# Kernel tuning notes

Measured on AMD Instinct MI355X. Metric: run time of the kernel, lower is better.

## Reference

```python
import jax, jax.numpy as jnp
import numpy as np

B, N, DIM = 4, 4096, 512
HEADS, DH = 8, 64          # dim_head = dim // 8
M = 256                    # num_landmarks = dim // 2
ITERS = 6                  # pinv iterations
K = 33                     # residual depthwise conv kernel
INNER = HEADS * DH


def setup_inputs() -> dict:
    key = jax.random.key(0)
    ks = jax.random.split(key, 7)
    return {
        "x": jax.random.normal(ks[0], (B, N, DIM), jnp.float32),
        "norm_w": 1.0 + 0.02 * jax.random.normal(ks[1], (DIM,), jnp.float32),
        "norm_b": 0.02 * jax.random.normal(ks[2], (DIM,), jnp.float32),
        "w_qkv": jax.random.normal(ks[3], (DIM, 3 * INNER), jnp.float32) / np.sqrt(DIM),
        "w_out": jax.random.normal(ks[4], (INNER, DIM), jnp.float32) / np.sqrt(INNER),
        "b_out": 0.02 * jax.random.normal(ks[5], (DIM,), jnp.float32),
        "res_w": jax.random.normal(ks[6], (HEADS, 1, K, 1), jnp.float32) / np.sqrt(K),
    }


def _moore_penrose_pinv(x, iters):
    # iterative Newton-Schulz pseudoinverse, as in lucidrains nystrom-attention
    abs_x = jnp.abs(x)
    col = abs_x.sum(-1)
    row = abs_x.sum(-2)
    z = jnp.swapaxes(x, -1, -2) / (jnp.max(col) * jnp.max(row))
    I = jnp.eye(x.shape[-1], dtype=x.dtype)
    for _ in range(iters):
        xz = x @ z
        z = 0.25 * z @ (13.0 * I - xz @ (15.0 * I - xz @ (7.0 * I - xz)))
    return z


def reference(x, norm_w, norm_b, w_qkv, w_out, b_out, res_w):
    # LayerNorm (eps=1e-5, torch default)
    mu = x.mean(-1, keepdims=True)
    var = ((x - mu) ** 2).mean(-1, keepdims=True)
    xn = (x - mu) / jnp.sqrt(var + 1e-5) * norm_w + norm_b

    qkv = xn @ w_qkv                               # [B,N,3*INNER]
    q, k, v = jnp.split(qkv, 3, axis=-1)
    to_heads = lambda t: t.reshape(B, N, HEADS, DH).transpose(0, 2, 1, 3)  # [B,H,N,D]
    q, k, v = to_heads(q), to_heads(k), to_heads(v)
    q = q * (DH ** -0.5)

    # landmarks: mean over consecutive blocks of l = N // M tokens
    l = N // M
    q_l = q.reshape(B, HEADS, M, l, DH).mean(3)    # [B,H,M,D]
    k_l = k.reshape(B, HEADS, M, l, DH).mean(3)

    sim1 = jnp.einsum('bhid,bhjd->bhij', q, k_l)   # [B,H,N,M]
    sim2 = jnp.einsum('bhid,bhjd->bhij', q_l, k_l) # [B,H,M,M]
    sim3 = jnp.einsum('bhid,bhjd->bhij', q_l, k)   # [B,H,M,N]
    a1 = jax.nn.softmax(sim1, -1)
    a2 = jax.nn.softmax(sim2, -1)
    a3 = jax.nn.softmax(sim3, -1)

    a2_inv = _moore_penrose_pinv(a2, ITERS)
    out = (a1 @ a2_inv) @ (a3 @ v)                 # [B,H,N,D]

    # residual depthwise conv over sequence dim (Conv2d(h,h,(33,1),groups=h))
    out = out + jax.lax.conv_general_dilated(
        v, res_w, (1, 1), ((K // 2, K // 2), (0, 0)),
        feature_group_count=HEADS,
        dimension_numbers=('NCHW', 'OIHW', 'NCHW'))

    out = out.transpose(0, 2, 1, 3).reshape(B, N, INNER)
    out = out @ w_out + b_out                      # to_out (dropout inactive at eval)
    return x + out                                 # TransLayer residual
```

## Files before the change

kernel.cpp:

```cpp
#include <hip/hip_runtime.h>
#include <math.h>

typedef unsigned short u16;
typedef short s16x8 __attribute__((ext_vector_type(8)));
typedef float f32x4 __attribute__((ext_vector_type(4)));

#define MFMA16(a, b, c) __builtin_amdgcn_mfma_f32_16x16x32_bf16((a), (b), (c), 0, 0, 0)

__device__ __forceinline__ u16 f2b(float f) {
  unsigned u = __float_as_uint(f);
  unsigned r = (u + 0x7fff + ((u >> 16) & 1)) >> 16;
  return (u16)r;
}
__device__ __forceinline__ float b2f(u16 h) { return __uint_as_float(((unsigned)h) << 16); }

__global__ __launch_bounds__(256) void ln_kernel(const float* __restrict__ x, const float* __restrict__ w,
                          const float* __restrict__ b, u16* __restrict__ xn) {
  int row = blockIdx.x;
  const float* xr = x + (size_t)row * 512;
  int t = threadIdx.x;
  float v0 = xr[t], v1 = xr[t + 256];
  float s = v0 + v1, ss = v0*v0 + v1*v1;
  for (int o = 32; o > 0; o >>= 1) { s += __shfl_down(s, o); ss += __shfl_down(ss, o); }
  __shared__ float ls[4], lss[4];
  int wid = t >> 6, lane = t & 63;
  if (lane == 0) { ls[wid] = s; lss[wid] = ss; }
  __syncthreads();
  float tot  = ls[0]+ls[1]+ls[2]+ls[3];
  float tot2 = lss[0]+lss[1]+lss[2]+lss[3];
  float mean = tot * (1.f/512);
  float var  = tot2 * (1.f/512) - mean*mean;
  float inv = rsqrtf(var + 1e-5f);
  u16* xo = xn + (size_t)row * 512;
  xo[t]     = f2b((v0-mean)*inv*w[t]     + b[t]);
  xo[t+256] = f2b((v1-mean)*inv*w[t+256] + b[t+256]);
}

__global__ __launch_bounds__(256) void wcast_T(const float* __restrict__ W, u16* __restrict__ WT, int R, int C) {
  int idx = blockIdx.x*256 + threadIdx.x;
  if (idx >= R*C) return;
  int r = idx / C, c = idx - r*C;
  WT[(size_t)c*R + r] = f2b(W[idx]);
}

__global__ __launch_bounds__(256) void vtrans(const u16* __restrict__ v, u16* __restrict__ vT) {
  __shared__ u16 tile[64][72];
  int bh = blockIdx.y, n0 = blockIdx.x * 64;
  int t = threadIdx.x;
  const u16* vb = v + ((size_t)bh*4096 + n0)*64;
  #pragma unroll
  for (int p = 0; p < 2; p++) {
    int c = t + p*256;
    int r = c >> 3, col = (c & 7)*8;
    *(uint4*)&tile[r][col] = *(const uint4*)&vb[(size_t)r*64 + col];
  }
  __syncthreads();
  #pragma unroll
  for (int p = 0; p < 2; p++) {
    int c = t + p*256;
    int d = c >> 3, ncol = (c & 7)*8;
    u16 tmp[8];
    #pragma unroll
    for (int j = 0; j < 8; j++) tmp[j] = tile[ncol + j][d];
    *(uint4*)&vT[((size_t)bh*64 + d)*4096 + n0 + ncol] = *(uint4*)tmp;
  }
}

__device__ __forceinline__ void gemm128_pf(const u16* __restrict__ A, const u16* __restrict__ BT,
    int K, int ldA, int ldBT, int row0, int col0, u16* As, u16* Bs, f32x4 acc[4][4]) {
  int t = threadIdx.x, lane = t & 63, wid = t >> 6;
  int wr = (wid >> 1) * 64, wc = (wid & 1) * 64;
  int lr = lane & 15, lg = lane >> 4;
  int sr = t >> 2, sc = (t & 3) * 8;
  const u16* Ar0 = A  + (size_t)(row0 + sr)*ldA + sc;
  const u16* Ar1 = A  + (size_t)(row0 + sr + 64)*ldA + sc;
  const u16* Br0 = BT + (size_t)(col0 + sr)*ldBT + sc;
  const u16* Br1 = BT + (size_t)(col0 + sr + 64)*ldBT + sc;
  uint4 pa0 = *(const uint4*)Ar0, pa1 = *(const uint4*)Ar1;
  uint4 pb0 = *(const uint4*)Br0, pb1 = *(const uint4*)Br1;
  for (int k0 = 0; k0 < K; k0 += 32) {
    __syncthreads();
    *(uint4*)&As[sr*40 + sc]        = pa0;
    *(uint4*)&As[(sr + 64)*40 + sc] = pa1;
    *(uint4*)&Bs[sr*40 + sc]        = pb0;
    *(uint4*)&Bs[(sr + 64)*40 + sc] = pb1;
    __syncthreads();
    if (k0 + 32 < K) {
      pa0 = *(const uint4*)(Ar0 + k0 + 32);
      pa1 = *(const uint4*)(Ar1 + k0 + 32);
      pb0 = *(const uint4*)(Br0 + k0 + 32);
      pb1 = *(const uint4*)(Br1 + k0 + 32);
    }
    s16x8 af[4], bf[4];
    #pragma unroll
    for (int f = 0; f < 4; f++) {
      af[f] = *(s16x8*)&As[(wr + f*16 + lr)*40 + lg*8];
      bf[f] = *(s16x8*)&Bs[(wc + f*16 + lr)*40 + lg*8];
    }
    #pragma unroll
    for (int i = 0; i < 4; i++)
      #pragma unroll
      for (int j = 0; j < 4; j++)
        acc[i][j] = MFMA16(af[i], bf[j], acc[i][j]);
  }
}

__device__ __forceinline__ void gemm64_pf(const u16* __restrict__ Ab, const u16* __restrict__ Bb,
    int row0, int col0, u16* As, u16* Bs, f32x4 acc[2][2]) {
  int t = threadIdx.x, lane = t & 63, wid = t >> 6;
  int wr = (wid >> 1)*32, wc = (wid & 1)*32;
  int lr = lane & 15, lg = lane >> 4;
  int sr = t >> 3, sc = (t & 7)*8;
  const u16* Ar0 = Ab + (size_t)(row0 + sr)*256 + sc;
  const u16* Ar1 = Ab + (size_t)(row0 + 32 + sr)*256 + sc;
  const u16* Br0 = Bb + (size_t)(col0 + sr)*256 + sc;
  const u16* Br1 = Bb + (size_t)(col0 + 32 + sr)*256 + sc;
  uint4 pa0 = *(const uint4*)Ar0, pa1 = *(const uint4*)Ar1;
  uint4 pb0 = *(const uint4*)Br0, pb1 = *(const uint4*)Br1;
  for (int k0 = 0; k0 < 256; k0 += 64) {
    __syncthreads();
    *(uint4*)&As[sr*72 + sc]        = pa0;
    *(uint4*)&As[(sr + 32)*72 + sc] = pa1;
    *(uint4*)&Bs[sr*72 + sc]        = pb0;
    *(uint4*)&Bs[(sr + 32)*72 + sc] = pb1;
    __syncthreads();
    if (k0 + 64 < 256) {
      pa0 = *(const uint4*)(Ar0 + k0 + 64);
      pa1 = *(const uint4*)(Ar1 + k0 + 64);
      pb0 = *(const uint4*)(Br0 + k0 + 64);
      pb1 = *(const uint4*)(Br1 + k0 + 64);
    }
    #pragma unroll
    for (int kk = 0; kk < 2; kk++) {
      s16x8 af[2], bf[2];
      #pragma unroll
      for (int f = 0; f < 2; f++) {
        af[f] = *(s16x8*)&As[(wr + f*16 + lr)*72 + kk*32 + lg*8];
        bf[f] = *(s16x8*)&Bs[(wc + f*16 + lr)*72 + kk*32 + lg*8];
      }
      #pragma unroll
      for (int i = 0; i < 2; i++)
        #pragma unroll
        for (int j = 0; j < 2; j++)
          acc[i][j] = MFMA16(af[i], bf[j], acc[i][j]);
    }
  }
}

__global__ __launch_bounds__(256, 4) void qkv_mfma(const u16* __restrict__ xn, const u16* __restrict__ wT,
    u16* __restrict__ q, u16* __restrict__ k, u16* __restrict__ v) {
  __shared__ u16 As[128*40], Bs[128*40];
  f32x4 acc[4][4];
  #pragma unroll
  for (int i = 0; i < 4; i++)
    #pragma unroll
    for (int j = 0; j < 4; j++) acc[i][j] = (f32x4)0.f;
  int bI = blockIdx.x;
  int job = (bI & 7)*192 + (bI >> 3);
  int row0 = (job / 12) * 128, col0 = (job % 12) * 128;
  gemm128_pf(xn, wT, 512, 512, 512, row0, col0, As, Bs, acc);
  int t = threadIdx.x, lane = t & 63, wid = t >> 6, lr = lane & 15, lg = lane >> 4;
  int wr = (wid >> 1)*64, wc = (wid & 1)*64;
  #pragma unroll
  for (int i = 0; i < 4; i++)
    #pragma unroll
    for (int j = 0; j < 4; j++)
      #pragma unroll
      for (int r = 0; r < 4; r++) {
        int row = row0 + wr + i*16 + lg*4 + r;
        int col = col0 + wc + j*16 + lr;
        float val = acc[i][j][r];
        int part = col >> 9, rem = col & 511, h = rem >> 6, d = rem & 63;
        int b = row >> 12, n = row & 4095;
        size_t bh = (size_t)(b*8 + h);
        size_t dst = (bh*4096 + n)*64 + d;
        if (part == 0)      q[dst] = f2b(val * 0.125f);
        else if (part == 1) k[dst] = f2b(val);
        else                v[dst] = f2b(val);
      }
}

__global__ __launch_bounds__(256, 4) void out_mfma(const u16* __restrict__ outh, const u16* __restrict__ wT,
    const float* __restrict__ bo, const float* __restrict__ x, float* __restrict__ out) {
  __shared__ u16 As[128*40], Bs[128*40];
  f32x4 acc[4][4];
  #pragma unroll
  for (int i = 0; i < 4; i++)
    #pragma unroll
    for (int j = 0; j < 4; j++) acc[i][j] = (f32x4)0.f;
  int bI = blockIdx.x;
  int job = (bI & 7)*64 + (bI >> 3);
  int row0 = (job / 4) * 128, col0 = (job % 4) * 128;
  gemm128_pf(outh, wT, 512, 512, 512, row0, col0, As, Bs, acc);
  int t = threadIdx.x, lane = t & 63, wid = t >> 6, lr = lane & 15, lg = lane >> 4;
  int wr = (wid >> 1)*64, wc = (wid & 1)*64;
  #pragma unroll
  for (int i = 0; i < 4; i++)
    #pragma unroll
    for (int j = 0; j < 4; j++)
      #pragma unroll
      for (int r = 0; r < 4; r++) {
        int row = row0 + wr + i*16 + lg*4 + r;
        int col = col0 + wc + j*16 + lr;
        size_t idx = (size_t)row*512 + col;
        out[idx] = x[idx] + acc[i][j][r] + bo[col];
      }
}

__global__ __launch_bounds__(256) void pinv_s1(const u16* __restrict__ a2h, const u16* __restrict__ zcT,
    u16* __restrict__ xz, u16* __restrict__ xzT, u16* __restrict__ e1T) {
  __shared__ u16 As[64*72], Bs[64*72];
  size_t bb = (size_t)blockIdx.z << 16;
  f32x4 acc[2][2];
  #pragma unroll
  for (int i = 0; i < 2; i++) { acc[i][0] = (f32x4)0.f; acc[i][1] = (f32x4)0.f; }
  int row0 = blockIdx.y*64, col0 = blockIdx.x*64;
  gemm64_pf(a2h + bb, zcT + bb, row0, col0, As, Bs, acc);
  int t = threadIdx.x, lane = t & 63, wid = t >> 6, lr = lane & 15, lg = lane >> 4;
  int wr = (wid >> 1)*32, wc = (wid & 1)*32;
  #pragma unroll
  for (int i = 0; i < 2; i++)
    #pragma unroll
    for (int j = 0; j < 2; j++)
      #pragma unroll
      for (int r = 0; r < 4; r++) {
        int row = row0 + wr + i*16 + lg*4 + r;
        int col = col0 + wc + j*16 + lr;
        float c = acc[i][j][r];
        xz [bb + (size_t)row*256 + col] = f2b(c);
        xzT[bb + (size_t)col*256 + row] = f2b(c);
        e1T[bb + (size_t)col*256 + row] = f2b((row == col ? 7.f : 0.f) - c);
      }
}

__global__ __launch_bounds__(256) void pinv_s2(const u16* __restrict__ xz, const u16* __restrict__ e1T,
    const u16* __restrict__ zc, const u16* __restrict__ xzT,
    u16* __restrict__ e2T, u16* __restrict__ W) {
  __shared__ u16 As[64*72], Bs[64*72];
  int bz = blockIdx.z;
  bool isQ = bz < 32;
  size_t bb = (size_t)(isQ ? bz : bz - 32) << 16;
  const u16* Aptr = (isQ ? xz : zc) + bb;
  const u16* Bptr = (isQ ? e1T : xzT) + bb;
  f32x4 acc[2][2];
  #pragma unroll
  for (int i = 0; i < 2; i++) { acc[i][0] = (f32x4)0.f; acc[i][1] = (f32x4)0.f; }
  int row0 = blockIdx.y*64, col0 = blockIdx.x*64;
  gemm64_pf(Aptr, Bptr, row0, col0, As, Bs, acc);
  int t = threadIdx.x, lane = t & 63, wid = t >> 6, lr = lane & 15, lg = lane >> 4;
  int wr = (wid >> 1)*32, wc = (wid & 1)*32;
  #pragma unroll
  for (int i = 0; i < 2; i++)
    #pragma unroll
    for (int j = 0; j < 2; j++)
      #pragma unroll
      for (int r = 0; r < 4; r++) {
        int row = row0 + wr + i*16 + lg*4 + r;
        int col = col0 + wc + j*16 + lr;
        float c = acc[i][j][r];
        if (isQ) e2T[bb + (size_t)col*256 + row] = f2b((row == col ? 15.f : 0.f) - c);
        else     W  [bb + (size_t)row*256 + col] = f2b(c);
      }
}

__global__ __launch_bounds__(256) void pinv_s3(const u16* __restrict__ W, const u16* __restrict__ e2T,
    const u16* __restrict__ zc, u16* __restrict__ zn, u16* __restrict__ znT) {
  __shared__ u16 As[64*72], Bs[64*72];
  size_t bb = (size_t)blockIdx.z << 16;
  f32x4 acc[2][2];
  #pragma unroll
  for (int i = 0; i < 2; i++) { acc[i][0] = (f32x4)0.f; acc[i][1] = (f32x4)0.f; }
  int row0 = blockIdx.y*64, col0 = blockIdx.x*64;
  gemm64_pf(W + bb, e2T + bb, row0, col0, As, Bs, acc);
  int t = threadIdx.x, lane = t & 63, wid = t >> 6, lr = lane & 15, lg = lane >> 4;
  int wr = (wid >> 1)*32, wc = (wid & 1)*32;
  #pragma unroll
  for (int i = 0; i < 2; i++)
    #pragma unroll
    for (int j = 0; j < 2; j++)
      #pragma unroll
      for (int r = 0; r < 4; r++) {
        int row = row0 + wr + i*16 + lg*4 + r;
        int col = col0 + wc + j*16 + lr;
        size_t idx = bb + (size_t)row*256 + col;
        float val = 3.25f*b2f(zc[idx]) - 0.25f*acc[i][j][r];
        zn [idx] = f2b(val);
        znT[bb + (size_t)col*256 + row] = f2b(val);
      }
}

__global__ __launch_bounds__(256) void bmm64(const u16* __restrict__ A, const u16* __restrict__ BT,
    u16* __restrict__ CT, int M, int N, int K) {
  __shared__ u16 As[64*40], Bs[64*40];
  int batch = blockIdx.z;
  const u16* Ab = A  + (size_t)batch*M*K;
  const u16* Bb = BT + (size_t)batch*N*K;
  int row0 = blockIdx.y*64, col0 = blockIdx.x*64;
  int t = threadIdx.x, lane = t & 63, wid = t >> 6, lr = lane & 15, lg = lane >> 4;
  int wr = (wid >> 1)*32, wc = (wid & 1)*32;
  int sr = t >> 2, sc = (t & 3)*8;
  const u16* Arow = Ab + (size_t)(row0 + sr)*K + sc;
  const u16* Brow = Bb + (size_t)(col0 + sr)*K + sc;
  uint4 pa = *(const uint4*)Arow;
  uint4 pb = *(const uint4*)Brow;
  f32x4 acc[2][2];
  #pragma unroll
  for (int i = 0; i < 2; i++)
    #pragma unroll
    for (int j = 0; j < 2; j++) acc[i][j] = (f32x4)0.f;
  for (int k0 = 0; k0 < K; k0 += 32) {
    __syncthreads();
    *(uint4*)&As[sr*40 + sc] = pa;
    *(uint4*)&Bs[sr*40 + sc] = pb;
    __syncthreads();
    if (k0 + 32 < K) {
      pa = *(const uint4*)(Arow + k0 + 32);
      pb = *(const uint4*)(Brow + k0 + 32);
    }
    s16x8 af[2], bf[2];
    #pragma unroll
    for (int f = 0; f < 2; f++) {
      af[f] = *(s16x8*)&As[(wr + f*16 + lr)*40 + lg*8];
      bf[f] = *(s16x8*)&Bs[(wc + f*16 + lr)*40 + lg*8];
    }
    #pragma unroll
    for (int i = 0; i < 2; i++)
      #pragma unroll
      for (int j = 0; j < 2; j++)
        acc[i][j] = MFMA16(af[i], bf[j], acc[i][j]);
  }
  size_t cb = (size_t)batch*M*N;
  #pragma unroll
  for (int i = 0; i < 2; i++)
    #pragma unroll
    for (int j = 0; j < 2; j++)
      #pragma unroll
      for (int r = 0; r < 4; r++) {
        int row = row0 + wr + i*16 + lg*4 + r;
        int col = col0 + wc + j*16 + lr;
        CT[cb + (size_t)col*M + row] = f2b(acc[i][j][r]);
      }
}

__global__ void landmark_kernel(const u16* __restrict__ q, const u16* __restrict__ k,
                                u16* __restrict__ ql, u16* __restrict__ kl) {
  int idx = blockIdx.x;
  int d = threadIdx.x;
  size_t base = ((size_t)idx * 16) * 64 + d;
  float sq = 0.f, sk = 0.f;
  #pragma unroll
  for (int j = 0; j < 16; j++) { sq += b2f(q[base + (size_t)j*64]); sk += b2f(k[base + (size_t)j*64]); }
  ql[(size_t)idx*64 + d] = f2b(sq * (1.f/16.f));
  kl[(size_t)idx*64 + d] = f2b(sk * (1.f/16.f));
}

__global__ __launch_bounds__(256, 4) void sim2_mfma(const u16* __restrict__ ql, const u16* __restrict__ kl,
    float* __restrict__ a2, u16* __restrict__ a2h, float* __restrict__ pcs) {
  __shared__ u16 Qs[64*72];
  __shared__ u16 Ks2[256*72];
  __shared__ float wcol[4*256];
  int rq = blockIdx.x, bh = blockIdx.y;
  int t = threadIdx.x, lane = t & 63, wid = t >> 6, lr = lane & 15, lg = lane >> 4;
  #pragma unroll
  for (int p = 0; p < 2; p++) {
    int c = t + p*256;
    int r = c >> 3, col = (c & 7)*8;
    *(uint4*)&Qs[r*72 + col] = *(const uint4*)&ql[((size_t)bh*256 + rq*64 + r)*64 + col];
  }
  #pragma unroll
  for (int p = 0; p < 8; p++) {
    int c = t + p*256;
    int r = c >> 3, col = (c & 7)*8;
    *(uint4*)&Ks2[r*72 + col] = *(const uint4*)&kl[((size_t)bh*256 + r)*64 + col];
  }
  __syncthreads();
  float colp[16];
  #pragma unroll
  for (int cf = 0; cf < 16; cf++) colp[cf] = 0.f;
  int rbase = wid*16;
  s16x8 a0 = *(s16x8*)&Qs[(rbase + lr)*72 + lg*8];
  s16x8 a1 = *(s16x8*)&Qs[(rbase + lr)*72 + 32 + lg*8];
  f32x4 sf[16];
  #pragma unroll
  for (int cf = 0; cf < 16; cf++) {
    s16x8 b0 = *(s16x8*)&Ks2[(cf*16 + lr)*72 + lg*8];
    s16x8 b1 = *(s16x8*)&Ks2[(cf*16 + lr)*72 + 32 + lg*8];
    sf[cf] = MFMA16(a1, b1, MFMA16(a0, b0, (f32x4)0.f));
  }
  #pragma unroll
  for (int r = 0; r < 4; r++) {
    float mx = -3e38f;
    #pragma unroll
    for (int cf = 0; cf < 16; cf++) mx = fmaxf(mx, sf[cf][r]);
    #pragma unroll
    for (int o = 1; o < 16; o <<= 1) mx = fmaxf(mx, __shfl_xor(mx, o));
    float sum = 0.f;
    #pragma unroll
    for (int cf = 0; cf < 16; cf++) { sf[cf][r] = __expf(sf[cf][r] - mx); sum += sf[cf][r]; }
    #pragma unroll
    for (int o = 1; o < 16; o <<= 1) sum += __shfl_xor(sum, o);
    float inv = 1.f / sum;
    int row = rq*64 + rbase + lg*4 + r;
    size_t base = (size_t)bh*65536 + (size_t)row*256;
    #pragma unroll
    for (int cf = 0; cf < 16; cf++) {
      float pp = sf[cf][r] * inv;
      a2[base + cf*16 + lr] = pp;
      a2h[base + cf*16 + lr] = f2b(pp);
      colp[cf] += pp;
    }
  }
  #pragma unroll
  for (int cf = 0; cf < 16; cf++) {
    colp[cf] += __shfl_xor(colp[cf], 16);
    colp[cf] += __shfl_xor(colp[cf], 32);
  }
  if (lg == 0) {
    #pragma unroll
    for (int cf = 0; cf < 16; cf++) wcol[wid*256 + cf*16 + lr] = colp[cf];
  }
  __syncthreads();
  pcs[((size_t)bh*4 + rq)*256 + t] = wcol[t] + wcol[256 + t] + wcol[512 + t] + wcol[768 + t];
}

__global__ __launch_bounds__(256) void colmax_kernel(const float* __restrict__ pcs, unsigned* __restrict__ scal) {
  __shared__ float red[256];
  int bh = blockIdx.x, t = threadIdx.x;
  size_t b4 = (size_t)bh*4*256;
  red[t] = pcs[b4 + t] + pcs[b4 + 256 + t] + pcs[b4 + 512 + t] + pcs[b4 + 768 + t];
  __syncthreads();
  for (int o = 128; o > 0; o >>= 1) {
    if (t < o) red[t] = fmaxf(red[t], red[t+o]);
    __syncthreads();
  }
  if (t == 0) atomicMax(scal + 1, __float_as_uint(red[0]));
}

__global__ void z0_kernel(const float* __restrict__ a2, const unsigned* __restrict__ scal,
                          u16* __restrict__ zA, u16* __restrict__ zAT) {
  size_t idx = (size_t)blockIdx.x*256 + threadIdx.x;
  float inv = 1.f / __uint_as_float(scal[1]);
  size_t bh = idx >> 16; int rem = (int)(idx & 65535); int i = rem >> 8, j = rem & 255;
  zA[idx]  = f2b(a2[(bh<<16) + ((size_t)j<<8) + i] * inv);
  zAT[idx] = f2b(a2[idx] * inv);
}

__global__ __launch_bounds__(256) void flash_part(const u16* __restrict__ Q, const u16* __restrict__ Kg,
    const u16* __restrict__ VT, u16* __restrict__ po, float* __restrict__ pm, float* __restrict__ pl) {
  __shared__ u16 Ks[64*72];
  __shared__ u16 Vs[64*72];
  __shared__ u16 Ps[4*16*72];
  int qg = blockIdx.x, ch = blockIdx.y, bh = blockIdx.z;
  int t = threadIdx.x, lane = t & 63, wid = t >> 6, lr = lane & 15, lg = lane >> 4;
  const u16* Qb  = Q  + ((size_t)bh*256)*64;
  const u16* Kb  = Kg + ((size_t)bh*4096 + ch*512)*64;
  const u16* VTb = VT + ((size_t)bh*64)*4096 + ch*512;
  s16x8 aq[2][2];
  #pragma unroll
  for (int qq = 0; qq < 2; qq++) {
    int qrow = (qg*2 + qq)*64 + wid*16 + lr;
    aq[qq][0] = *(const s16x8*)&Qb[(size_t)qrow*64 + lg*8];
    aq[qq][1] = *(const s16x8*)&Qb[(size_t)qrow*64 + 32 + lg*8];
  }
  f32x4 oacc[2][4];
  float m_[2][4], l_[2][4];
  #pragma unroll
  for (int qq = 0; qq < 2; qq++)
    #pragma unroll
    for (int f = 0; f < 4; f++) {
      oacc[qq][f] = (f32x4)0.f;
      m_[qq][f] = -3e38f;
      l_[qq][f] = 0.f;
    }
  u16* Pw = Ps + wid*16*72;
  uint4 pk[2], pv[2];
  #pragma unroll
  for (int p = 0; p < 2; p++) {
    int c = t + p*256; int r = c >> 3, cc = (c & 7)*8;
    pk[p] = *(const uint4*)&Kb[(size_t)r*64 + cc];
    pv[p] = *(const uint4*)&VTb[(size_t)r*4096 + cc];
  }
  for (int k0 = 0; k0 < 512; k0 += 64) {
    __syncthreads();
    #pragma unroll
    for (int p = 0; p < 2; p++) {
      int c = t + p*256; int r = c >> 3, cc = (c & 7)*8;
      *(uint4*)&Ks[r*72 + cc] = pk[p];
      *(uint4*)&Vs[r*72 + cc] = pv[p];
    }
    __syncthreads();
    if (k0 + 64 < 512) {
      #pragma unroll
      for (int p = 0; p < 2; p++) {
        int c = t + p*256; int r = c >> 3, cc = (c & 7)*8;
        pk[p] = *(const uint4*)&Kb[(size_t)(k0 + 64 + r)*64 + cc];
        pv[p] = *(const uint4*)&VTb[(size_t)r*4096 + k0 + 64 + cc];
      }
    }
    #pragma unroll
    for (int qq = 0; qq < 2; qq++) {
      f32x4 sf[4];
      #pragma unroll
      for (int f = 0; f < 4; f++) {
        s16x8 b0 = *(s16x8*)&Ks[(f*16 + lr)*72 + lg*8];
        s16x8 b1 = *(s16x8*)&Ks[(f*16 + lr)*72 + 32 + lg*8];
        f32x4 s = (f32x4)0.f;
        s = MFMA16(aq[qq][0], b0, s);
        s = MFMA16(aq[qq][1], b1, s);
        sf[f] = s;
      }
      #pragma unroll
      for (int r = 0; r < 4; r++) {
        float mx = fmaxf(fmaxf(sf[0][r], sf[1][r]), fmaxf(sf[2][r], sf[3][r]));
        #pragma unroll
        for (int o = 1; o < 16; o <<= 1) mx = fmaxf(mx, __shfl_xor(mx, o));
        float mn = fmaxf(m_[qq][r], mx);
        float sum = 0.f;
        #pragma unroll
        for (int f = 0; f < 4; f++) {
          float pv2 = __expf(sf[f][r] - mn);
          sum += pv2;
          Pw[(lg*4 + r)*72 + f*16 + lr] = f2b(pv2);
        }
        #pragma unroll
        for (int o = 1; o < 16; o <<= 1) sum += __shfl_xor(sum, o);
        float sc = __expf(m_[qq][r] - mn);
        l_[qq][r] = l_[qq][r]*sc + sum;
        m_[qq][r] = mn;
        #pragma unroll
        for (int f = 0; f < 4; f++) oacc[qq][f][r] *= sc;
      }
      #pragma unroll
      for (int ks = 0; ks < 2; ks++) {
        s16x8 ap = *(s16x8*)&Pw[lr*72 + ks*32 + lg*8];
        #pragma unroll
        for (int df = 0; df < 4; df++) {
          s16x8 bv = *(s16x8*)&Vs[(df*16 + lr)*72 + ks*32 + lg*8];
          oacc[qq][df] = MFMA16(ap, bv, oacc[qq][df]);
        }
      }
    }
  }
  #pragma unroll
  for (int qq = 0; qq < 2; qq++) {
    int pidx = (bh*4 + qg*2 + qq)*8 + ch;
    #pragma unroll
    for (int r = 0; r < 4; r++) {
      int lrow = wid*16 + lg*4 + r;
      if (lr == 0) { pm[pidx*64 + lrow] = m_[qq][r]; pl[pidx*64 + lrow] = l_[qq][r]; }
      uint2 pw2;
      pw2.x = (unsigned)f2b(oacc[qq][0][r]) | ((unsigned)f2b(oacc[qq][1][r]) << 16);
      pw2.y = (unsigned)f2b(oacc[qq][2][r]) | ((unsigned)f2b(oacc[qq][3][r]) << 16);
      *(uint2*)&po[((size_t)pidx*64 + lrow)*64 + lr*4] = pw2;
    }
  }
}

__global__ __launch_bounds__(256) void flash_merge(const u16* __restrict__ po, const float* __restrict__ pm,
    const float* __restrict__ pl, u16* __restrict__ a3vT) {
  __shared__ u16 tile[64*72];
  int qt = blockIdx.x, bh = blockIdx.y;
  int t = threadIdx.x;
  int lrow = t & 63, dg = t >> 6;
  int pbase = (bh*4 + qt)*8;
  float m = -3e38f;
  #pragma unroll
  for (int ch = 0; ch < 8; ch++) m = fmaxf(m, pm[(pbase+ch)*64 + lrow]);
  float w[8];
  float L = 0.f;
  #pragma unroll
  for (int ch = 0; ch < 8; ch++) {
    w[ch] = __expf(pm[(pbase+ch)*64 + lrow] - m);
    L += w[ch] * pl[(pbase+ch)*64 + lrow];
  }
  float Oacc[16];
  #pragma unroll
  for (int ss = 0; ss < 16; ss++) Oacc[ss] = 0.f;
  #pragma unroll
  for (int ch = 0; ch < 8; ch++) {
    const u16* pr = &po[(((size_t)(pbase+ch)*64 + lrow)*64) + dg*16];
    uint4 v0 = *(const uint4*)pr;
    uint4 v1 = *(const uint4*)(pr + 8);
    float wc = w[ch];
    unsigned arr[8] = {v0.x, v0.y, v0.z, v0.w, v1.x, v1.y, v1.z, v1.w};
    #pragma unroll
    for (int jj = 0; jj < 8; jj++) {
      Oacc[jj*2]   += wc * b2f((u16)(arr[jj] & 0xffff));
      Oacc[jj*2+1] += wc * b2f((u16)(arr[jj] >> 16));
    }
  }
  float Linv = 1.f / L;
  #pragma unroll
  for (int ss = 0; ss < 16; ss++) {
    int s = dg*16 + ss;
    int c = ((s & 3) << 4) | (s >> 2);
    tile[c*72 + lrow] = f2b(Oacc[ss] * Linv);
  }
  __syncthreads();
  #pragma unroll
  for (int p = 0; p < 2; p++) {
    int idx = t + p*256;
    int d = idx >> 3, seg = idx & 7;
    u16 tmp[8];
    #pragma unroll
    for (int j = 0; j < 8; j++) tmp[j] = tile[d*72 + seg*8 + j];
    *(uint4*)&a3vT[((size_t)bh*64 + d)*256 + qt*64 + seg*8] = *(uint4*)tmp;
  }
}

__global__ __launch_bounds__(256, 4) void flash_a1(const u16* __restrict__ Q, const u16* __restrict__ Kl,
    const u16* __restrict__ W2T, u16* __restrict__ outh) {
  __shared__ u16 Ks[64*72];
  __shared__ u16 Vs[64*264];
  __shared__ u16 Ps[4*16*264];
  int bh = blockIdx.y;
  int q0 = blockIdx.x * 64;
  int t = threadIdx.x, lane = t & 63, wid = t >> 6, lr = lane & 15, lg = lane >> 4;
  const u16* Qb = Q + ((size_t)bh*4096)*64;
  #pragma unroll
  for (int p = 0; p < 8; p++) {
    int c = t + p*256; int r = c >> 5, col = (c & 31)*8;
    *(uint4*)&Vs[r*264 + col] = *(const uint4*)&W2T[((size_t)bh*64 + r)*256 + col];
  }
  int qrow = q0 + wid*16 + lr;
  s16x8 aq0 = *(const s16x8*)&Qb[(size_t)qrow*64 + lg*8];
  s16x8 aq1 = *(const s16x8*)&Qb[(size_t)qrow*64 + 32 + lg*8];
  f32x4 sf[16];
  #pragma unroll
  for (int f = 0; f < 16; f++) sf[f] = (f32x4)0.f;
  #pragma unroll
  for (int kt = 0; kt < 4; kt++) {
    __syncthreads();
    #pragma unroll
    for (int p = 0; p < 2; p++) {
      int c = t + p*256; int r = c >> 3, cc = (c & 7)*8;
      *(uint4*)&Ks[r*72 + cc] = *(const uint4*)&Kl[((size_t)bh*256 + kt*64 + r)*64 + cc];
    }
    __syncthreads();
    #pragma unroll
    for (int f2 = 0; f2 < 4; f2++) {
      s16x8 b0 = *(s16x8*)&Ks[(f2*16 + lr)*72 + lg*8];
      s16x8 b1 = *(s16x8*)&Ks[(f2*16 + lr)*72 + 32 + lg*8];
      sf[kt*4 + f2] = MFMA16(aq1, b1, MFMA16(aq0, b0, sf[kt*4 + f2]));
    }
  }
  u16* Pw = Ps + wid*16*264;
  float linv[4];
  #pragma unroll
  for (int r = 0; r < 4; r++) {
    float mx = -3e38f;
    #pragma unroll
    for (int f = 0; f < 16; f++) mx = fmaxf(mx, sf[f][r]);
    #pragma unroll
    for (int o = 1; o < 16; o <<= 1) mx = fmaxf(mx, __shfl_xor(mx, o));
    float sum = 0.f;
    #pragma unroll
    for (int f = 0; f < 16; f++) {
      float pv = __expf(sf[f][r] - mx);
      sum += pv;
      Pw[(lg*4 + r)*264 + f*16 + lr] = f2b(pv);
    }
    #pragma unroll
    for (int o = 1; o < 16; o <<= 1) sum += __shfl_xor(sum, o);
    linv[r] = 1.f / sum;
  }
  f32x4 oacc[4];
  #pragma unroll
  for (int f = 0; f < 4; f++) oacc[f] = (f32x4)0.f;
  #pragma unroll
  for (int ks = 0; ks < 8; ks++) {
    s16x8 ap = *(s16x8*)&Pw[lr*264 + ks*32 + lg*8];
    #pragma unroll
    for (int df = 0; df < 4; df++) {
      s16x8 bv = *(s16x8*)&Vs[(df*16 + lr)*264 + ks*32 + lg*8];
      oacc[df] = MFMA16(ap, bv, oacc[df]);
    }
  }
  int b = bh >> 3, h = bh & 7;
  #pragma unroll
  for (int df = 0; df < 4; df++)
    #pragma unroll
    for (int r = 0; r < 4; r++) {
      int lrow = wid*16 + lg*4 + r;
      int col = df*16 + lr;
      outh[((size_t)(b*4096 + q0 + lrow))*512 + h*64 + col] = f2b(oacc[df][r] * linv[r]);
    }
}

__global__ __launch_bounds__(256) void conv_lds(const u16* __restrict__ v, const float* __restrict__ rw,
                                                u16* __restrict__ outh) {
  __shared__ u16 tile[160*72];
  __shared__ float wsm[33];
  int bh = blockIdx.y;
  int n0 = blockIdx.x * 128;
  int b = bh >> 3, h = bh & 7;
  int t = threadIdx.x;
  if (t < 33) wsm[t] = rw[h*33 + t];
  const u16* vb = v + ((size_t)bh*4096)*64;
  #pragma unroll
  for (int p = 0; p < 5; p++) {
    int c = t + p*256;
    int r = c >> 3, col = (c & 7)*8;
    int nn = n0 - 16 + r;
    uint4 val = make_uint4(0u,0u,0u,0u);
    if (nn >= 0 && nn < 4096) val = *(const uint4*)&vb[(size_t)nn*64 + col];
    *(uint4*)&tile[r*72 + col] = val;
  }
  __syncthreads();
  int d8 = (t & 7) * 8;
  int r0 = t >> 3;
  #pragma unroll
  for (int pass = 0; pass < 4; pass++) {
    int lrow = pass*32 + r0;
    float acc[8] = {};
    #pragma unroll
    for (int j = 0; j < 33; j++) {
      uint4 vv = *(uint4*)&tile[(lrow + j)*72 + d8];
      float w = wsm[j];
      acc[0] += b2f((u16)(vv.x & 0xffff)) * w;
      acc[1] += b2f((u16)(vv.x >> 16))    * w;
      acc[2] += b2f((u16)(vv.y & 0xffff)) * w;
      acc[3] += b2f((u16)(vv.y >> 16))    * w;
      acc[4] += b2f((u16)(vv.z & 0xffff)) * w;
      acc[5] += b2f((u16)(vv.z >> 16))    * w;
      acc[6] += b2f((u16)(vv.w & 0xffff)) * w;
      acc[7] += b2f((u16)(vv.w >> 16))    * w;
    }
    size_t oi = ((size_t)(b*4096 + n0 + lrow))*512 + h*64 + d8;
    uint4 ov = *(uint4*)&outh[oi];
    uint4 nv;
    nv.x = (unsigned)f2b(b2f((u16)(ov.x & 0xffff)) + acc[0]) | ((unsigned)f2b(b2f((u16)(ov.x >> 16)) + acc[1]) << 16);
    nv.y = (unsigned)f2b(b2f((u16)(ov.y & 0xffff)) + acc[2]) | ((unsigned)f2b(b2f((u16)(ov.y >> 16)) + acc[3]) << 16);
    nv.z = (unsigned)f2b(b2f((u16)(ov.z & 0xffff)) + acc[4]) | ((unsigned)f2b(b2f((u16)(ov.z >> 16)) + acc[5]) << 16);
    nv.w = (unsigned)f2b(b2f((u16)(ov.w & 0xffff)) + acc[6]) | ((unsigned)f2b(b2f((u16)(ov.w >> 16)) + acc[7]) << 16);
    *(uint4*)&outh[oi] = nv;
  }
}

extern "C" void kernel_launch(void* const* d_in, const int* in_sizes, int n_in,
                              void* d_out, int out_size, void* d_ws, size_t ws_size,
                              hipStream_t stream) {
  const float* x      = (const float*)d_in[0];
  const float* norm_w = (const float*)d_in[1];
  const float* norm_b = (const float*)d_in[2];
  const float* w_qkv  = (const float*)d_in[3];
  const float* w_out  = (const float*)d_in[4];
  const float* b_out  = (const float*)d_in[5];
  const float* res_w  = (const float*)d_in[6];
  float* out = (float*)d_out;
  char* ws = (char*)d_ws;

  size_t off = 0;
  u16* xn    = (u16*)(ws + off); off += 16777216;
  u16* q     = (u16*)(ws + off); off += 16777216;
  u16* k     = (u16*)(ws + off); off += 16777216;
  u16* v     = (u16*)(ws + off); off += 16777216;
  u16* vT    = (u16*)(ws + off); off += 16777216;
  u16* ql    = (u16*)(ws + off); off += 1048576;
  u16* kl    = (u16*)(ws + off); off += 1048576;
  float* a2  = (float*)(ws + off); off += 8388608;
  u16* a2h   = (u16*)(ws + off); off += 4194304;
  u16* zA    = (u16*)(ws + off); off += 4194304;
  u16* zAT   = (u16*)(ws + off); off += 4194304;
  u16* zB    = (u16*)(ws + off); off += 4194304;
  u16* zBT   = (u16*)(ws + off); off += 4194304;
  u16* xz    = (u16*)(ws + off); off += 4194304;
  u16* xzT   = (u16*)(ws + off); off += 4194304;
  u16* e1T   = (u16*)(ws + off); off += 4194304;
  u16* e2T   = (u16*)(ws + off); off += 4194304;
  u16* Wm    = (u16*)(ws + off); off += 4194304;
  u16* a3vT  = (u16*)(ws + off); off += 1048576;
  u16* w2T   = (u16*)(ws + off); off += 1048576;
  u16* wqkvT = (u16*)(ws + off); off += 1572864;
  u16* woutT = (u16*)(ws + off); off += 524288;
  u16* outh  = (u16*)(ws + off); off += 16777216;
  u16* po    = (u16*)(ws + off); off += 8388608;
  float* pm  = (float*)(ws + off); off += 262144;
  float* pl  = (float*)(ws + off); off += 262144;
  float* pcs = (float*)(ws + off); off += 131072;
  unsigned* scal = (unsigned*)(ws + off); off += 8;

  ln_kernel<<<16384, 256, 0, stream>>>(x, norm_w, norm_b, xn);
  wcast_T<<<3072, 256, 0, stream>>>(w_qkv, wqkvT, 512, 1536);
  wcast_T<<<1024, 256, 0, stream>>>(w_out, woutT, 512, 512);
  qkv_mfma<<<1536, 256, 0, stream>>>(xn, wqkvT, q, k, v);
  vtrans<<<dim3(64, 32), 256, 0, stream>>>(v, vT);
  landmark_kernel<<<8192, 64, 0, stream>>>(q, k, ql, kl);
  hipMemsetAsync(scal, 0, 8, stream);
  sim2_mfma<<<dim3(4, 32), 256, 0, stream>>>(ql, kl, a2, a2h, pcs);
  colmax_kernel<<<32, 256, 0, stream>>>(pcs, scal);
  flash_part<<<dim3(2, 8, 32), 256, 0, stream>>>(ql, k, vT, po, pm, pl);
  flash_merge<<<dim3(4, 32), 256, 0, stream>>>(po, pm, pl, a3vT);
  z0_kernel<<<8192, 256, 0, stream>>>(a2, scal, zA, zAT);

  u16 *zc = zA, *zcT = zAT, *zn = zB, *znT = zBT;
  for (int it = 0; it < 6; it++) {
    pinv_s1<<<dim3(4,4,32), 256, 0, stream>>>(a2h, zcT, xz, xzT, e1T);
    pinv_s2<<<dim3(4,4,64), 256, 0, stream>>>(xz, e1T, zc, xzT, e2T, Wm);
    pinv_s3<<<dim3(4,4,32), 256, 0, stream>>>(Wm, e2T, zc, zn, znT);
    u16* tp;
    tp = zc; zc = zn; zn = tp;
    tp = zcT; zcT = znT; znT = tp;
  }

  bmm64<<<dim3(1,4,32), 256, 0, stream>>>(zc, a3vT, w2T, 256, 64, 256);
  flash_a1<<<dim3(64, 32), 256, 0, stream>>>(q, kl, w2T, outh);
  conv_lds<<<dim3(32, 32), 256, 0, stream>>>(v, res_w, outh);
  out_mfma<<<512, 256, 0, stream>>>(outh, woutT, b_out, x, out);
}
```

Measured before the change: 421.8 us.

## Merge small launches, deepen GEMM prefetch, and make flash rescale conditional

Combines several independent small kernels into shared launches: LayerNorm with both weight cast-transposes, the V transpose with landmark averaging, and the flash merge with the z0 initialization. The goal is to cut per-launch overhead and idle gaps between tiny kernels. The 128x128 GEMM helper now prefetches two K-steps ahead from global memory using double register buffers, which costs extra registers. The flash_part online softmax only rescales the accumulators when the running max actually increases.

```diff
diff --git a/kernel.cpp b/kernel.cpp
--- a/kernel.cpp
+++ b/kernel.cpp
@@ -14,59 +14,79 @@
 }
 __device__ __forceinline__ float b2f(u16 h) { return __uint_as_float(((unsigned)h) << 16); }
 
-__global__ __launch_bounds__(256) void ln_kernel(const float* __restrict__ x, const float* __restrict__ w,
-                          const float* __restrict__ b, u16* __restrict__ xn) {
-  int row = blockIdx.x;
-  const float* xr = x + (size_t)row * 512;
+__global__ __launch_bounds__(256) void prep_kernel(const float* __restrict__ x, const float* __restrict__ w,
+    const float* __restrict__ b, u16* __restrict__ xn,
+    const float* __restrict__ Wq, u16* __restrict__ WqT,
+    const float* __restrict__ Wo, u16* __restrict__ WoT) {
+  int bI = blockIdx.x;
   int t = threadIdx.x;
-  float v0 = xr[t], v1 = xr[t + 256];
-  float s = v0 + v1, ss = v0*v0 + v1*v1;
-  for (int o = 32; o > 0; o >>= 1) { s += __shfl_down(s, o); ss += __shfl_down(ss, o); }
-  __shared__ float ls[4], lss[4];
-  int wid = t >> 6, lane = t & 63;
-  if (lane == 0) { ls[wid] = s; lss[wid] = ss; }
-  __syncthreads();
-  float tot  = ls[0]+ls[1]+ls[2]+ls[3];
-  float tot2 = lss[0]+lss[1]+lss[2]+lss[3];
-  float mean = tot * (1.f/512);
-  float var  = tot2 * (1.f/512) - mean*mean;
-  float inv = rsqrtf(var + 1e-5f);
-  u16* xo = xn + (size_t)row * 512;
-  xo[t]     = f2b((v0-mean)*inv*w[t]     + b[t]);
-  xo[t+256] = f2b((v1-mean)*inv*w[t+256] + b[t+256]);
-}
-
-__global__ __launch_bounds__(256) void wcast_T(const float* __restrict__ W, u16* __restrict__ WT, int R, int C) {
-  int idx = blockIdx.x*256 + threadIdx.x;
-  if (idx >= R*C) return;
-  int r = idx / C, c = idx - r*C;
-  WT[(size_t)c*R + r] = f2b(W[idx]);
-}
-
-__global__ __launch_bounds__(256) void vtrans(const u16* __restrict__ v, u16* __restrict__ vT) {
+  if (bI < 16384) {
+    int row = bI;
+    const float* xr = x + (size_t)row * 512;
+    float v0 = xr[t], v1 = xr[t + 256];
+    float s = v0 + v1, ss = v0*v0 + v1*v1;
+    for (int o = 32; o > 0; o >>= 1) { s += __shfl_down(s, o); ss += __shfl_down(ss, o); }
+    __shared__ float ls[4], lss[4];
+    int wid = t >> 6, lane = t & 63;
+    if (lane == 0) { ls[wid] = s; lss[wid] = ss; }
+    __syncthreads();
+    float tot  = ls[0]+ls[1]+ls[2]+ls[3];
+    float tot2 = lss[0]+lss[1]+lss[2]+lss[3];
+    float mean = tot * (1.f/512);
+    float var  = tot2 * (1.f/512) - mean*mean;
+    float inv = rsqrtf(var + 1e-5f);
+    u16* xo = xn + (size_t)row * 512;
+    xo[t]     = f2b((v0-mean)*inv*w[t]     + b[t]);
+    xo[t+256] = f2b((v1-mean)*inv*w[t+256] + b[t+256]);
+  } else if (bI < 16384 + 3072) {
+    int idx = (bI - 16384)*256 + t;
+    int r = idx / 1536, c = idx - r*1536;
+    WqT[(size_t)c*512 + r] = f2b(Wq[idx]);
+  } else {
+    int idx = (bI - 19456)*256 + t;
+    int r = idx >> 9, c = idx & 511;
+    WoT[(size_t)c*512 + r] = f2b(Wo[idx]);
+  }
+}
+
+__global__ __launch_bounds__(256) void vt_lm(const u16* __restrict__ v, u16* __restrict__ vT,
+    const u16* __restrict__ q, const u16* __restrict__ k,
+    u16* __restrict__ ql, u16* __restrict__ kl) {
   __shared__ u16 tile[64][72];
-  int bh = blockIdx.y, n0 = blockIdx.x * 64;
+  int bI = blockIdx.x;
   int t = threadIdx.x;
-  const u16* vb = v + ((size_t)bh*4096 + n0)*64;
-  #pragma unroll
-  for (int p = 0; p < 2; p++) {
-    int c = t + p*256;
-    int r = c >> 3, col = (c & 7)*8;
-    *(uint4*)&tile[r][col] = *(const uint4*)&vb[(size_t)r*64 + col];
-  }
-  __syncthreads();
-  #pragma unroll
-  for (int p = 0; p < 2; p++) {
-    int c = t + p*256;
-    int d = c >> 3, ncol = (c & 7)*8;
-    u16 tmp[8];
-    #pragma unroll
-    for (int j = 0; j < 8; j++) tmp[j] = tile[ncol + j][d];
-    *(uint4*)&vT[((size_t)bh*64 + d)*4096 + n0 + ncol] = *(uint4*)tmp;
-  }
-}
-
-__device__ __forceinline__ void gemm128_pf(const u16* __restrict__ A, const u16* __restrict__ BT,
+  if (bI < 2048) {
+    int bh = bI >> 6, n0 = (bI & 63) * 64;
+    const u16* vb = v + ((size_t)bh*4096 + n0)*64;
+    #pragma unroll
+    for (int p = 0; p < 2; p++) {
+      int c = t + p*256;
+      int r = c >> 3, col = (c & 7)*8;
+      *(uint4*)&tile[r][col] = *(const uint4*)&vb[(size_t)r*64 + col];
+    }
+    __syncthreads();
+    #pragma unroll
+    for (int p = 0; p < 2; p++) {
+      int c = t + p*256;
+      int d = c >> 3, ncol = (c & 7)*8;
+      u16 tmp[8];
+      #pragma unroll
+      for (int j = 0; j < 8; j++) tmp[j] = tile[ncol + j][d];
+      *(uint4*)&vT[((size_t)bh*64 + d)*4096 + n0 + ncol] = *(uint4*)tmp;
+    }
+  } else {
+    int idx = (bI - 2048)*4 + (t >> 6);
+    int d = t & 63;
+    size_t base = ((size_t)idx * 16) * 64 + d;
+    float sq = 0.f, sk = 0.f;
+    #pragma unroll
+    for (int j = 0; j < 16; j++) { sq += b2f(q[base + (size_t)j*64]); sk += b2f(k[base + (size_t)j*64]); }
+    ql[(size_t)idx*64 + d] = f2b(sq * (1.f/16.f));
+    kl[(size_t)idx*64 + d] = f2b(sk * (1.f/16.f));
+  }
+}
+
+__device__ __forceinline__ void gemm128_pf2(const u16* __restrict__ A, const u16* __restrict__ BT,
     int K, int ldA, int ldBT, int row0, int col0, u16* As, u16* Bs, f32x4 acc[4][4]) {
   int t = threadIdx.x, lane = t & 63, wid = t >> 6;
   int wr = (wid >> 1) * 64, wc = (wid & 1) * 64;
@@ -76,20 +96,27 @@
   const u16* Ar1 = A  + (size_t)(row0 + sr + 64)*ldA + sc;
   const u16* Br0 = BT + (size_t)(col0 + sr)*ldBT + sc;
   const u16* Br1 = BT + (size_t)(col0 + sr + 64)*ldBT + sc;
-  uint4 pa0 = *(const uint4*)Ar0, pa1 = *(const uint4*)Ar1;
-  uint4 pb0 = *(const uint4*)Br0, pb1 = *(const uint4*)Br1;
+  uint4 pa0[2], pa1[2], pb0[2], pb1[2];
+  #pragma unroll
+  for (int s = 0; s < 2; s++) {
+    pa0[s] = *(const uint4*)(Ar0 + s*32);
+    pa1[s] = *(const uint4*)(Ar1 + s*32);
+    pb0[s] = *(const uint4*)(Br0 + s*32);
+    pb1[s] = *(const uint4*)(Br1 + s*32);
+  }
   for (int k0 = 0; k0 < K; k0 += 32) {
-    __syncthreads();
-    *(uint4*)&As[sr*40 + sc]        = pa0;
-    *(uint4*)&As[(sr + 64)*40 + sc] = pa1;
-    *(uint4*)&Bs[sr*40 + sc]        = pb0;
-    *(uint4*)&Bs[(sr + 64)*40 + sc] = pb1;
-    __syncthreads();
-    if (k0 + 32 < K) {
-      pa0 = *(const uint4*)(Ar0 + k0 + 32);
-      pa1 = *(const uint4*)(Ar1 + k0 + 32);
-      pb0 = *(const uint4*)(Br0 + k0 + 32);
-      pb1 = *(const uint4*)(Br1 + k0 + 32);
+    int s = (k0 >> 5) & 1;
+    __syncthreads();
+    *(uint4*)&As[sr*40 + sc]        = pa0[s];
+    *(uint4*)&As[(sr + 64)*40 + sc] = pa1[s];
+    *(uint4*)&Bs[sr*40 + sc]        = pb0[s];
+    *(uint4*)&Bs[(sr + 64)*40 + sc] = pb1[s];
+    __syncthreads();
+    if (k0 + 64 < K) {
+      pa0[s] = *(const uint4*)(Ar0 + k0 + 64);
+      pa1[s] = *(const uint4*)(Ar1 + k0 + 64);
+      pb0[s] = *(const uint4*)(Br0 + k0 + 64);
+      pb1[s] = *(const uint4*)(Br1 + k0 + 64);
     }
     s16x8 af[4], bf[4];
     #pragma unroll
@@ -158,7 +185,7 @@
   int bI = blockIdx.x;
   int job = (bI & 7)*192 + (bI >> 3);
   int row0 = (job / 12) * 128, col0 = (job % 12) * 128;
-  gemm128_pf(xn, wT, 512, 512, 512, row0, col0, As, Bs, acc);
+  gemm128_pf2(xn, wT, 512, 512, 512, row0, col0, As, Bs, acc);
   int t = threadIdx.x, lane = t & 63, wid = t >> 6, lr = lane & 15, lg = lane >> 4;
   int wr = (wid >> 1)*64, wc = (wid & 1)*64;
   #pragma unroll
@@ -191,7 +218,7 @@
   int bI = blockIdx.x;
   int job = (bI & 7)*64 + (bI >> 3);
   int row0 = (job / 4) * 128, col0 = (job % 4) * 128;
-  gemm128_pf(outh, wT, 512, 512, 512, row0, col0, As, Bs, acc);
+  gemm128_pf2(outh, wT, 512, 512, 512, row0, col0, As, Bs, acc);
   int t = threadIdx.x, lane = t & 63, wid = t >> 6, lr = lane & 15, lg = lane >> 4;
   int wr = (wid >> 1)*64, wc = (wid & 1)*64;
   #pragma unroll
@@ -342,18 +369,6 @@
       }
 }
 
-__global__ void landmark_kernel(const u16* __restrict__ q, const u16* __restrict__ k,
-                                u16* __restrict__ ql, u16* __restrict__ kl) {
-  int idx = blockIdx.x;
-  int d = threadIdx.x;
-  size_t base = ((size_t)idx * 16) * 64 + d;
-  float sq = 0.f, sk = 0.f;
-  #pragma unroll
-  for (int j = 0; j < 16; j++) { sq += b2f(q[base + (size_t)j*64]); sk += b2f(k[base + (size_t)j*64]); }
-  ql[(size_t)idx*64 + d] = f2b(sq * (1.f/16.f));
-  kl[(size_t)idx*64 + d] = f2b(sk * (1.f/16.f));
-}
-
 __global__ __launch_bounds__(256, 4) void sim2_mfma(const u16* __restrict__ ql, const u16* __restrict__ kl,
     float* __restrict__ a2, u16* __restrict__ a2h, float* __restrict__ pcs) {
   __shared__ u16 Qs[64*72];
@@ -434,15 +449,6 @@
     __syncthreads();
   }
   if (t == 0) atomicMax(scal + 1, __float_as_uint(red[0]));
-}
-
-__global__ void z0_kernel(const float* __restrict__ a2, const unsigned* __restrict__ scal,
-                          u16* __restrict__ zA, u16* __restrict__ zAT) {
-  size_t idx = (size_t)blockIdx.x*256 + threadIdx.x;
-  float inv = 1.f / __uint_as_float(scal[1]);
-  size_t bh = idx >> 16; int rem = (int)(idx & 65535); int i = rem >> 8, j = rem & 255;
-  zA[idx]  = f2b(a2[(bh<<16) + ((size_t)j<<8) + i] * inv);
-  zAT[idx] = f2b(a2[idx] * inv);
 }
 
 __global__ __launch_bounds__(256) void flash_part(const u16* __restrict__ Q, const u16* __restrict__ Kg,
@@ -514,7 +520,15 @@
         float mx = fmaxf(fmaxf(sf[0][r], sf[1][r]), fmaxf(sf[2][r], sf[3][r]));
         #pragma unroll
         for (int o = 1; o < 16; o <<= 1) mx = fmaxf(mx, __shfl_xor(mx, o));
-        float mn = fmaxf(m_[qq][r], mx);
+        float mn = m_[qq][r];
+        if (mx > mn) {
+          float sc = __expf(mn - mx);
+          l_[qq][r] *= sc;
+          #pragma unroll
+          for (int f = 0; f < 4; f++) oacc[qq][f][r] *= sc;
+          mn = mx;
+          m_[qq][r] = mx;
+        }
         float sum = 0.f;
         #pragma unroll
         for (int f = 0; f < 4; f++) {
@@ -524,11 +538,7 @@
         }
         #pragma unroll
         for (int o = 1; o < 16; o <<= 1) sum += __shfl_xor(sum, o);
-        float sc = __expf(m_[qq][r] - mn);
-        l_[qq][r] = l_[qq][r]*sc + sum;
-        m_[qq][r] = mn;
-        #pragma unroll
-        for (int f = 0; f < 4; f++) oacc[qq][f][r] *= sc;
+        l_[qq][r] += sum;
       }
       #pragma unroll
       for (int ks = 0; ks < 2; ks++) {
@@ -556,55 +566,66 @@
   }
 }
 
-__global__ __launch_bounds__(256) void flash_merge(const u16* __restrict__ po, const float* __restrict__ pm,
-    const float* __restrict__ pl, u16* __restrict__ a3vT) {
+__global__ __launch_bounds__(256) void merge_z0(const u16* __restrict__ po, const float* __restrict__ pm,
+    const float* __restrict__ pl, u16* __restrict__ a3vT,
+    const float* __restrict__ a2, const unsigned* __restrict__ scal,
+    u16* __restrict__ zA, u16* __restrict__ zAT) {
   __shared__ u16 tile[64*72];
-  int qt = blockIdx.x, bh = blockIdx.y;
+  int bI = blockIdx.x;
   int t = threadIdx.x;
-  int lrow = t & 63, dg = t >> 6;
-  int pbase = (bh*4 + qt)*8;
-  float m = -3e38f;
-  #pragma unroll
-  for (int ch = 0; ch < 8; ch++) m = fmaxf(m, pm[(pbase+ch)*64 + lrow]);
-  float w[8];
-  float L = 0.f;
-  #pragma unroll
-  for (int ch = 0; ch < 8; ch++) {
-    w[ch] = __expf(pm[(pbase+ch)*64 + lrow] - m);
-    L += w[ch] * pl[(pbase+ch)*64 + lrow];
-  }
-  float Oacc[16];
-  #pragma unroll
-  for (int ss = 0; ss < 16; ss++) Oacc[ss] = 0.f;
-  #pragma unroll
-  for (int ch = 0; ch < 8; ch++) {
-    const u16* pr = &po[(((size_t)(pbase+ch)*64 + lrow)*64) + dg*16];
-    uint4 v0 = *(const uint4*)pr;
-    uint4 v1 = *(const uint4*)(pr + 8);
-    float wc = w[ch];
-    unsigned arr[8] = {v0.x, v0.y, v0.z, v0.w, v1.x, v1.y, v1.z, v1.w};
-    #pragma unroll
-    for (int jj = 0; jj < 8; jj++) {
-      Oacc[jj*2]   += wc * b2f((u16)(arr[jj] & 0xffff));
-      Oacc[jj*2+1] += wc * b2f((u16)(arr[jj] >> 16));
-    }
-  }
-  float Linv = 1.f / L;
-  #pragma unroll
-  for (int ss = 0; ss < 16; ss++) {
-    int s = dg*16 + ss;
-    int c = ((s & 3) << 4) | (s >> 2);
-    tile[c*72 + lrow] = f2b(Oacc[ss] * Linv);
-  }
-  __syncthreads();
-  #pragma unroll
-  for (int p = 0; p < 2; p++) {
-    int idx = t + p*256;
-    int d = idx >> 3, seg = idx & 7;
-    u16 tmp[8];
-    #pragma unroll
-    for (int j = 0; j < 8; j++) tmp[j] = tile[d*72 + seg*8 + j];
-    *(uint4*)&a3vT[((size_t)bh*64 + d)*256 + qt*64 + seg*8] = *(uint4*)tmp;
+  if (bI < 128) {
+    int qt = bI & 3, bh = bI >> 2;
+    int lrow = t & 63, dg = t >> 6;
+    int pbase = (bh*4 + qt)*8;
+    float m = -3e38f;
+    #pragma unroll
+    for (int ch = 0; ch < 8; ch++) m = fmaxf(m, pm[(pbase+ch)*64 + lrow]);
+    float w[8];
+    float L = 0.f;
+    #pragma unroll
+    for (int ch = 0; ch < 8; ch++) {
+      w[ch] = __expf(pm[(pbase+ch)*64 + lrow] - m);
+      L += w[ch] * pl[(pbase+ch)*64 + lrow];
+    }
+    float Oacc[16];
+    #pragma unroll
+    for (int ss = 0; ss < 16; ss++) Oacc[ss] = 0.f;
+    #pragma unroll
+    for (int ch = 0; ch < 8; ch++) {
+      const u16* pr = &po[(((size_t)(pbase+ch)*64 + lrow)*64) + dg*16];
+      uint4 v0 = *(const uint4*)pr;
+      uint4 v1 = *(const uint4*)(pr + 8);
+      float wc = w[ch];
+      unsigned arr[8] = {v0.x, v0.y, v0.z, v0.w, v1.x, v1.y, v1.z, v1.w};
+      #pragma unroll
+      for (int jj = 0; jj < 8; jj++) {
+        Oacc[jj*2]   += wc * b2f((u16)(arr[jj] & 0xffff));
+        Oacc[jj*2+1] += wc * b2f((u16)(arr[jj] >> 16));
+      }
+    }
+    float Linv = 1.f / L;
+    #pragma unroll
+    for (int ss = 0; ss < 16; ss++) {
+      int s = dg*16 + ss;
+      int c = ((s & 3) << 4) | (s >> 2);
+      tile[c*72 + lrow] = f2b(Oacc[ss] * Linv);
+    }
+    __syncthreads();
+    #pragma unroll
+    for (int p = 0; p < 2; p++) {
+      int idx = t + p*256;
+      int d = idx >> 3, seg = idx & 7;
+      u16 tmp[8];
+      #pragma unroll
+      for (int j = 0; j < 8; j++) tmp[j] = tile[d*72 + seg*8 + j];
+      *(uint4*)&a3vT[((size_t)bh*64 + d)*256 + qt*64 + seg*8] = *(uint4*)tmp;
+    }
+  } else {
+    size_t idx = (size_t)(bI - 128)*256 + t;
+    float inv = 1.f / __uint_as_float(scal[1]);
+    size_t bh = idx >> 16; int rem = (int)(idx & 65535); int i = rem >> 8, j = rem & 255;
+    zA[idx]  = f2b(a2[(bh<<16) + ((size_t)j<<8) + i] * inv);
+    zAT[idx] = f2b(a2[idx] * inv);
   }
 }
 
@@ -780,18 +801,14 @@
   float* pcs = (float*)(ws + off); off += 131072;
   unsigned* scal = (unsigned*)(ws + off); off += 8;
 
-  ln_kernel<<<16384, 256, 0, stream>>>(x, norm_w, norm_b, xn);
-  wcast_T<<<3072, 256, 0, stream>>>(w_qkv, wqkvT, 512, 1536);
-  wcast_T<<<1024, 256, 0, stream>>>(w_out, woutT, 512, 512);
+  prep_kernel<<<20480, 256, 0, stream>>>(x, norm_w, norm_b, xn, w_qkv, wqkvT, w_out, woutT);
   qkv_mfma<<<1536, 256, 0, stream>>>(xn, wqkvT, q, k, v);
-  vtrans<<<dim3(64, 32), 256, 0, stream>>>(v, vT);
-  landmark_kernel<<<8192, 64, 0, stream>>>(q, k, ql, kl);
+  vt_lm<<<4096, 256, 0, stream>>>(v, vT, q, k, ql, kl);
   hipMemsetAsync(scal, 0, 8, stream);
   sim2_mfma<<<dim3(4, 32), 256, 0, stream>>>(ql, kl, a2, a2h, pcs);
   colmax_kernel<<<32, 256, 0, stream>>>(pcs, scal);
   flash_part<<<dim3(2, 8, 32), 256, 0, stream>>>(ql, k, vT, po, pm, pl);
-  flash_merge<<<dim3(4, 32), 256, 0, stream>>>(po, pm, pl, a3vT);
-  z0_kernel<<<8192, 256, 0, stream>>>(a2, scal, zA, zAT);
+  merge_z0<<<8320, 256, 0, stream>>>(po, pm, pl, a3vT, a2, scal, zA, zAT);
 
   u16 *zc = zA, *zcT = zAT, *zn = zB, *znT = zBT;
   for (int it = 0; it < 6; it++) {
```

After: 544.7 us. 29.1% more time.
